# Performance work log

Hardware: AMD Instinct MI355X
Metric: run time of the kernel (lower is better)

Reference implementation:

```python
import jax, jax.numpy as jnp
import numpy as np

SLOPE = 0.2  # LeakyReLU negative slope
EPS = 1e-8


def setup_inputs() -> dict:
    key = jax.random.key(0)
    ks = jax.random.split(key, 10)
    B, LL, D, H = 16, 257, 64, 128
    in_dim = D + 1  # lags=1 -> lags*D + 1
    sc = 0.1
    return {
        "x": jax.random.normal(ks[0], (B, LL, D), dtype=jnp.float32),
        "W1": jax.random.normal(ks[1], (D, H, in_dim), dtype=jnp.float32) * sc,
        "b1": jax.random.normal(ks[2], (D, H), dtype=jnp.float32) * sc,
        "W2": jax.random.normal(ks[3], (D, H, H), dtype=jnp.float32) * sc,
        "b2": jax.random.normal(ks[4], (D, H), dtype=jnp.float32) * sc,
        "W3": jax.random.normal(ks[5], (D, H, H), dtype=jnp.float32) * sc,
        "b3": jax.random.normal(ks[6], (D, H), dtype=jnp.float32) * sc,
        "W4": jax.random.normal(ks[7], (D, 1, H), dtype=jnp.float32) * sc,
        "b4": jax.random.normal(ks[8], (D, 1), dtype=jnp.float32) * sc,
        "lags": 1,
    }


def _forward(x, W1, b1, W2, b2, W3, b3, W4, b4, lags):
    B, LL, D = x.shape
    length = LL - lags
    # sliding windows of size lags+1 along time: [B, length, lags+1, D]
    windows = jnp.stack([x[:, i:i + length] for i in range(lags + 1)], axis=2)
    N = B * length
    x_lags = windows[:, :, :-1].reshape(N, lags * D)  # [N, lags*D]
    x_t = windows[:, :, -1].reshape(N, D)             # [N, D]

    def per_latent(w1, bb1, w2, bb2, w3, bb3, w4, bb4, xti):
        inp = jnp.concatenate([x_lags, xti[:, None]], axis=-1)  # [N, lags*D+1]
        p1 = inp @ w1.T + bb1
        s1 = jnp.where(p1 > 0, 1.0, SLOPE)
        a1 = p1 * s1
        p2 = a1 @ w2.T + bb2
        s2 = jnp.where(p2 > 0, 1.0, SLOPE)
        a2 = p2 * s2
        p3 = a2 @ w3.T + bb3
        s3 = jnp.where(p3 > 0, 1.0, SLOPE)
        a3 = p3 * s3
        out = a3 @ w4.T + bb4  # [N, 1]
        # analytic d out / d x_{t,i} (Jacobian diagonal): chain through LeakyReLU slopes
        d = s1 * w1[:, -1]      # [N, H]
        d = s2 * (d @ w2.T)     # [N, H]
        d = s3 * (d @ w3.T)     # [N, H]
        deriv = d @ w4[0]       # [N]
        return out[:, 0], deriv

    res, deriv = jax.vmap(per_latent, in_axes=(0, 0, 0, 0, 0, 0, 0, 0, 1))(
        W1, b1, W2, b2, W3, b3, W4, b4, x_t)  # res, deriv: [D, N]
    residuals = res.T.reshape(B, length, D)
    log_abs_det = jnp.log(jnp.abs(deriv) + EPS).sum(axis=0).reshape(B, length)
    return residuals, log_abs_det


def reference(x, W1, b1, W2, b2, W3, b3, W4, b4, lags):
    return _forward(x, W1, b1, W2, b2, W3, b3, W4, b4, lags)
```

## Files before the change

### kernel.cpp

```cpp
#include <hip/hip_runtime.h>
#include <hip/hip_bf16.h>
#include <math.h>

typedef _Float16 f16;
typedef _Float16 f16x8 __attribute__((ext_vector_type(8)));
typedef _Float16 f16x4 __attribute__((ext_vector_type(4)));
typedef _Float16 f16x2 __attribute__((ext_vector_type(2)));
typedef float f32x4 __attribute__((ext_vector_type(4)));

#define MFMA(a, b, c) __builtin_amdgcn_mfma_f32_16x16x32_f16((a), (b), (c), 0, 0, 0)

constexpr int Dd = 64;
constexpr int Hh = 128;
constexpr int Nn = 4096;
constexpr int NT = 32;
constexpr float SLP = 0.2f;
constexpr float INV2K = 1.0f / 2048.0f;

constexpr int PD = 81920;
constexpr size_t W1L_OFF = (size_t)Dd * PD * 2;
constexpr size_t WS_NEEDED = W1L_OFF + (size_t)Dd * Hh * 4;

__device__ __forceinline__ int swz(int r, int c) {
  return (r << 7) + ((((c >> 3) ^ (r & 15)) << 3) | (c & 7));
}
__device__ __forceinline__ int swzK64(int r, int c) {
  return (r << 6) + (((((c >> 3) ^ r) & 7) << 3) | (c & 7));
}
__device__ __forceinline__ int swzF(int n, int h) {
  return (n << 7) + ((((h >> 2) ^ n) & 31) << 2) + (h & 3);
}

struct HL { f16 h, l; };
__device__ __forceinline__ HL split(float v) {
  HL r;
  r.h = (f16)v;
  r.l = (f16)((v - (float)r.h) * 2048.0f);
  return r;
}

__device__ __forceinline__ void cp_lds_async(const void* g, void* l, int nbytes, int tid) {
  const int lane = tid & 63, wv = tid >> 6;
  for (int base = wv * 1024; base < nbytes; base += 4096) {
    __builtin_amdgcn_global_load_lds(
        (const __attribute__((address_space(1))) void*)((const char*)g + base + lane * 16),
        (__attribute__((address_space(3))) void*)((char*)l + base), 16, 0, 0);
  }
}

__global__ __launch_bounds__(256)
void prep_kernel(const float* __restrict__ W1, const float* __restrict__ W2,
                 const float* __restrict__ W3, f16* __restrict__ wsf,
                 float* __restrict__ w1lg) {
  const int d = blockIdx.x, sec = blockIdx.y, tid = threadIdx.x;
  f16* out = wsf + (size_t)d * PD;
  if (sec == 0) {
    const float* W1d = W1 + d * Hh * 65;
    for (int ip = tid; ip < 4096; ip += 256) {
      int h = ip >> 5, k2 = (ip & 31) << 1;
      HL a = split(W1d[h * 65 + k2]);
      HL b = split(W1d[h * 65 + k2 + 1]);
      int o = (h >> 6) * 8192 + swzK64(h & 63, k2);
      *(f16x2*)&out[o] = f16x2{a.h, b.h};
      *(f16x2*)&out[o + 4096] = f16x2{a.l, b.l};
    }
    if (tid < 128) w1lg[d * Hh + tid] = W1d[tid * 65 + 64];
  } else {
    int w = (sec - 1) >> 1, hh = (sec - 1) & 1;
    const float* g = (w == 0 ? W2 : W3) + d * Hh * Hh + hh * 8192;
    f16* ob = out + 16384 + w * 32768 + hh * 16384;
    for (int ip = tid; ip < 4096; ip += 256) {
      int h = ip >> 6, k2 = (ip & 63) << 1;
      float2 v = *(const float2*)&g[h * 128 + k2];
      HL a = split(v.x), b = split(v.y);
      int o = swz(h, k2);
      *(f16x2*)&ob[o] = f16x2{a.h, b.h};
      *(f16x2*)&ob[o + 8192] = f16x2{a.l, b.l};
    }
  }
}

__device__ __forceinline__ void mid_mfma_half(
    const f16* AH, const f16* AL, const f16* DH, const f16* DL,
    const f16* WH, const f16* WL, int nt, int wq, int l15, int quad,
    f32x4* aP, f32x4* aS, f32x4* dP, f32x4* dS) {
#pragma unroll
  for (int kc = 0; kc < 4; kc++) {
    int ko = kc * 32 + quad * 8;
    int ra = nt * 16 + l15;
    f16x8 xh = *(const f16x8*)&AH[swz(ra, ko)];
    f16x8 xl = *(const f16x8*)&AL[swz(ra, ko)];
    f16x8 yh = *(const f16x8*)&DH[swz(ra, ko)];
    f16x8 yl = *(const f16x8*)&DL[swz(ra, ko)];
#pragma unroll
    for (int c2 = 0; c2 < 2; c2++) {
      int hr = (2 * wq + c2) * 16 + l15;
      f16x8 wh = *(const f16x8*)&WH[swz(hr, ko)];
      f16x8 wl = *(const f16x8*)&WL[swz(hr, ko)];
      aP[c2] = MFMA(wh, xh, aP[c2]);
      aS[c2] = MFMA(wl, xh, aS[c2]);
      aS[c2] = MFMA(wh, xl, aS[c2]);
      dP[c2] = MFMA(wh, yh, dP[c2]);
      dS[c2] = MFMA(wl, yh, dS[c2]);
      dS[c2] = MFMA(wh, yl, dS[c2]);
    }
  }
}

__global__ __launch_bounds__(256, 2)
void np_prior_fast(const float* __restrict__ x, const f16* __restrict__ wsw,
                   const float* __restrict__ w1lg,
                   const float* __restrict__ b1, const float* __restrict__ b2,
                   const float* __restrict__ b3, const float* __restrict__ W4,
                   const float* __restrict__ b4,
                   float* __restrict__ out_res, float* __restrict__ out_log) {
  __shared__ float4 smem[4096];
  f16* AH = (f16*)smem;
  f16* AL = AH + NT * 128;
  f16* DH = AL + NT * 128;
  f16* DL = DH + NT * 128;
  f16* Wreg = (f16*)((char*)smem + 32768);
  float* A3F = (float*)smem;
  float* D3F = (float*)((char*)smem + 16384);

  const int tid = threadIdx.x, d = blockIdx.y, n0 = blockIdx.x * NT;
  const int lane = tid & 63, wv = tid >> 6, l15 = lane & 15, quad = lane >> 4;
  const int nt = wv & 1, wq = wv >> 1;

  const f16* wd = wsw + (size_t)d * PD;
  const float* w1l = w1lg + d * Hh;
  const float* b1d = b1 + d * Hh;
  const f32x4 zero = {0.f, 0.f, 0.f, 0.f};

  cp_lds_async(wd, Wreg, 16384, tid);

  for (int i = tid; i < NT * 16; i += 256) {
    int n = i >> 4, k4 = (i & 15) << 2;
    int ng = n0 + n, bb = ng >> 8, tt = ng & 255;
    float4 v = *(const float4*)&x[(bb * 257 + tt) * 64 + k4];
    HL a = split(v.x), b = split(v.y), c = split(v.z), e = split(v.w);
    int o = swz(n, k4);
    *(f16x4*)&AH[o] = f16x4{a.h, b.h, c.h, e.h};
    *(f16x4*)&AL[o] = f16x4{a.l, b.l, c.l, e.l};
  }
  float xtv;
  {
    int ng = n0 + nt * 16 + l15, bb = ng >> 8, tt = ng & 255;
    xtv = x[(bb * 257 + tt + 1) * 64 + d];
  }
  __syncthreads();

  f32x4 l1P[2][2], l1S[2][2];
  for (int hf = 0; hf < 2; hf++) {
    if (hf == 1) {
      __syncthreads();
      cp_lds_async(wd + 8192, Wreg, 16384, tid);
      __syncthreads();
    }
    l1P[hf][0] = zero; l1P[hf][1] = zero;
    l1S[hf][0] = zero; l1S[hf][1] = zero;
#pragma unroll
    for (int kc = 0; kc < 2; kc++) {
      int ko = kc * 32 + quad * 8;
      f16x8 xh = *(const f16x8*)&AH[swz(nt * 16 + l15, ko)];
      f16x8 xl = *(const f16x8*)&AL[swz(nt * 16 + l15, ko)];
#pragma unroll
      for (int c2 = 0; c2 < 2; c2++) {
        int hr = (2 * wq + c2) * 16 + l15;
        f16x8 wh = *(const f16x8*)&Wreg[swzK64(hr, ko)];
        f16x8 wl = *(const f16x8*)&Wreg[4096 + swzK64(hr, ko)];
        l1P[hf][c2] = MFMA(wh, xh, l1P[hf][c2]);
        l1S[hf][c2] = MFMA(wl, xh, l1S[hf][c2]);
        l1S[hf][c2] = MFMA(wh, xl, l1S[hf][c2]);
      }
    }
  }
  __syncthreads();
  cp_lds_async(wd + 16384, Wreg, 32768, tid);

  {
    int n = nt * 16 + l15;
#pragma unroll
    for (int hf = 0; hf < 2; hf++)
#pragma unroll
      for (int c2 = 0; c2 < 2; c2++) {
        int hb = hf * 64 + (2 * wq + c2) * 16 + quad * 4;
        float4 wv4 = *(const float4*)&w1l[hb];
        float4 bv4 = *(const float4*)&b1d[hb];
        f16x4 ah, al, dh, dl;
#pragma unroll
        for (int j = 0; j < 4; j++) {
          float w1j = (&wv4.x)[j];
          float p = l1P[hf][c2][j] + l1S[hf][c2][j] * INV2K + xtv * w1j + (&bv4.x)[j];
          float s = p > 0.f ? 1.f : SLP;
          HL av = split(p * s), dv = split(s * w1j);
          ah[j] = av.h; al[j] = av.l; dh[j] = dv.h; dl[j] = dv.l;
        }
        int o = swz(n, hb);
        *(f16x4*)&AH[o] = ah; *(f16x4*)&AL[o] = al;
        *(f16x4*)&DH[o] = dh; *(f16x4*)&DL[o] = dl;
      }
  }
  __syncthreads();

  f32x4 aP[2][2], aS[2][2], dP[2][2], dS[2][2];
  for (int hf = 0; hf < 2; hf++) {
    if (hf == 1) {
      __syncthreads();
      cp_lds_async(wd + 32768, Wreg, 32768, tid);
      __syncthreads();
    }
    aP[hf][0] = zero; aP[hf][1] = zero; aS[hf][0] = zero; aS[hf][1] = zero;
    dP[hf][0] = zero; dP[hf][1] = zero; dS[hf][0] = zero; dS[hf][1] = zero;
    mid_mfma_half(AH, AL, DH, DL, Wreg, Wreg + 8192, nt, wq, l15, quad,
                  aP[hf], aS[hf], dP[hf], dS[hf]);
  }
  __syncthreads();
  cp_lds_async(wd + 49152, Wreg, 32768, tid);

  {
    const float* b2d = b2 + d * Hh;
    int n = nt * 16 + l15;
#pragma unroll
    for (int hf = 0; hf < 2; hf++)
#pragma unroll
      for (int c2 = 0; c2 < 2; c2++) {
        int hb = hf * 64 + (2 * wq + c2) * 16 + quad * 4;
        float4 bv4 = *(const float4*)&b2d[hb];
        f16x4 ah, al, dh, dl;
#pragma unroll
        for (int j = 0; j < 4; j++) {
          float p = aP[hf][c2][j] + aS[hf][c2][j] * INV2K + (&bv4.x)[j];
          float s = p > 0.f ? 1.f : SLP;
          float dd = s * (dP[hf][c2][j] + dS[hf][c2][j] * INV2K);
          HL av = split(p * s), dv = split(dd);
          ah[j] = av.h; al[j] = av.l; dh[j] = dv.h; dl[j] = dv.l;
        }
        int o = swz(n, hb);
        *(f16x4*)&AH[o] = ah; *(f16x4*)&AL[o] = al;
        *(f16x4*)&DH[o] = dh; *(f16x4*)&DL[o] = dl;
      }
  }
  __syncthreads();

  for (int hf = 0; hf < 2; hf++) {
    if (hf == 1) {
      __syncthreads();
      cp_lds_async(wd + 65536, Wreg, 32768, tid);
      __syncthreads();
    }
    aP[hf][0] = zero; aP[hf][1] = zero; aS[hf][0] = zero; aS[hf][1] = zero;
    dP[hf][0] = zero; dP[hf][1] = zero; dS[hf][0] = zero; dS[hf][1] = zero;
    mid_mfma_half(AH, AL, DH, DL, Wreg, Wreg + 8192, nt, wq, l15, quad,
                  aP[hf], aS[hf], dP[hf], dS[hf]);
  }
  __syncthreads();

  {
    const float* b3d = b3 + d * Hh;
    int n = nt * 16 + l15;
#pragma unroll
    for (int hf = 0; hf < 2; hf++)
#pragma unroll
      for (int c2 = 0; c2 < 2; c2++) {
        int hb = hf * 64 + (2 * wq + c2) * 16 + quad * 4;
        float4 bv4 = *(const float4*)&b3d[hb];
        float4 pa, pd;
#pragma unroll
        for (int j = 0; j < 4; j++) {
          float p = aP[hf][c2][j] + aS[hf][c2][j] * INV2K + (&bv4.x)[j];
          float s = p > 0.f ? 1.f : SLP;
          (&pa.x)[j] = p * s;
          (&pd.x)[j] = s * (dP[hf][c2][j] + dS[hf][c2][j] * INV2K);
        }
        *(float4*)&A3F[swzF(n, hb)] = pa;
        *(float4*)&D3F[swzF(n, hb)] = pd;
      }
  }
  __syncthreads();

  {
    int n = tid >> 3, oct = tid & 7;
    const float* w4d = W4 + d * Hh;
    float sr = 0.f, sd = 0.f;
#pragma unroll
    for (int i = 0; i < 4; i++) {
      int c = oct * 16 + i * 4;
      float4 va = *(const float4*)&A3F[swzF(n, c)];
      float4 vd = *(const float4*)&D3F[swzF(n, c)];
      float4 w = *(const float4*)&w4d[c];
      sr += va.x * w.x + va.y * w.y + va.z * w.z + va.w * w.w;
      sd += vd.x * w.x + vd.y * w.y + vd.z * w.z + vd.w * w.w;
    }
    sr += __shfl_xor(sr, 1); sr += __shfl_xor(sr, 2); sr += __shfl_xor(sr, 4);
    sd += __shfl_xor(sd, 1); sd += __shfl_xor(sd, 2); sd += __shfl_xor(sd, 4);
    if (oct == 0) {
      int ng = n0 + n;
      out_res[ng * 64 + d] = sr + b4[d];
      atomicAdd(&out_log[ng], logf(fabsf(sd) + 1e-8f));
    }
  }
}

__device__ __forceinline__ void stage_wf(f16* WH, f16* WL,
                                         const float* __restrict__ g, int tid) {
  for (int i = tid; i < 2048; i += 256) {
    int h = i >> 5, k4 = (i & 31) << 2;
    float4 v = ((const float4*)g)[i];
    HL a = split(v.x), b = split(v.y), c = split(v.z), e = split(v.w);
    int o = swz(h, k4);
    *(f16x4*)&WH[o] = f16x4{a.h, b.h, c.h, e.h};
    *(f16x4*)&WL[o] = f16x4{a.l, b.l, c.l, e.l};
  }
}

__global__ __launch_bounds__(256, 2)
void np_prior_fb(const float* __restrict__ x,
                 const float* __restrict__ W1, const float* __restrict__ b1,
                 const float* __restrict__ W2, const float* __restrict__ b2,
                 const float* __restrict__ W3, const float* __restrict__ b3,
                 const float* __restrict__ W4, const float* __restrict__ b4,
                 float* __restrict__ out_res, float* __restrict__ out_log) {
  __shared__ float4 smem[4096];
  f16* AH = (f16*)smem;
  f16* AL = AH + NT * 128;
  f16* DH = AL + NT * 128;
  f16* DL = DH + NT * 128;
  f16* WHp = (f16*)((char*)smem + 32768);
  f16* WLp = WHp + 64 * 128;
  float* A3F = (float*)smem;
  float* D3F = (float*)((char*)smem + 16384);

  const int tid = threadIdx.x, d = blockIdx.y, n0 = blockIdx.x * NT;
  const int lane = tid & 63, wv = tid >> 6, l15 = lane & 15, quad = lane >> 4;
  const int nt = wv & 1, wq = wv >> 1;

  const float* W1d = W1 + d * Hh * 65;
  const float* b1d = b1 + d * Hh;
  const f32x4 zero = {0.f, 0.f, 0.f, 0.f};

  for (int i = tid; i < NT * 16; i += 256) {
    int n = i >> 4, k4 = (i & 15) << 2;
    int ng = n0 + n, bb = ng >> 8, tt = ng & 255;
    float4 v = *(const float4*)&x[(bb * 257 + tt) * 64 + k4];
    HL a = split(v.x), b = split(v.y), c = split(v.z), e = split(v.w);
    int o = swz(n, k4);
    *(f16x4*)&AH[o] = f16x4{a.h, b.h, c.h, e.h};
    *(f16x4*)&AL[o] = f16x4{a.l, b.l, c.l, e.l};
  }
  float xtv;
  {
    int ng = n0 + nt * 16 + l15, bb = ng >> 8, tt = ng & 255;
    xtv = x[(bb * 257 + tt + 1) * 64 + d];
  }
  for (int i = tid; i < 64 * 64; i += 256) {
    int h = i >> 6, k = i & 63;
    HL s = split(W1d[h * 65 + k]);
    int o = swz(h, k);
    WHp[o] = s.h; WLp[o] = s.l;
  }
  __syncthreads();

  f32x4 l1P[2][2], l1S[2][2];
  for (int hf = 0; hf < 2; hf++) {
    if (hf == 1) {
      __syncthreads();
      for (int i = tid; i < 64 * 64; i += 256) {
        int h = i >> 6, k = i & 63;
        HL s = split(W1d[(64 + h) * 65 + k]);
        int o = swz(h, k);
        WHp[o] = s.h; WLp[o] = s.l;
      }
      __syncthreads();
    }
    l1P[hf][0] = zero; l1P[hf][1] = zero;
    l1S[hf][0] = zero; l1S[hf][1] = zero;
#pragma unroll
    for (int kc = 0; kc < 2; kc++) {
      int ko = kc * 32 + quad * 8;
      f16x8 xh = *(const f16x8*)&AH[swz(nt * 16 + l15, ko)];
      f16x8 xl = *(const f16x8*)&AL[swz(nt * 16 + l15, ko)];
#pragma unroll
      for (int c2 = 0; c2 < 2; c2++) {
        int hr = (2 * wq + c2) * 16 + l15;
        f16x8 wh = *(const f16x8*)&WHp[swz(hr, ko)];
        f16x8 wl = *(const f16x8*)&WLp[swz(hr, ko)];
        l1P[hf][c2] = MFMA(wh, xh, l1P[hf][c2]);
        l1S[hf][c2] = MFMA(wl, xh, l1S[hf][c2]);
        l1S[hf][c2] = MFMA(wh, xl, l1S[hf][c2]);
      }
    }
  }
  __syncthreads();

  {
    int n = nt * 16 + l15;
#pragma unroll
    for (int hf = 0; hf < 2; hf++)
#pragma unroll
      for (int c2 = 0; c2 < 2; c2++) {
        int hb = hf * 64 + (2 * wq + c2) * 16 + quad * 4;
        f16x4 ah, al, dh, dl;
#pragma unroll
        for (int j = 0; j < 4; j++) {
          int h = hb + j;
          float w1j = W1d[h * 65 + 64];
          float p = l1P[hf][c2][j] + l1S[hf][c2][j] * INV2K + xtv * w1j + b1d[h];
          float s = p > 0.f ? 1.f : SLP;
          HL av = split(p * s), dv = split(s * w1j);
          ah[j] = av.h; al[j] = av.l; dh[j] = dv.h; dl[j] = dv.l;
        }
        int o = swz(n, hb);
        *(f16x4*)&AH[o] = ah; *(f16x4*)&AL[o] = al;
        *(f16x4*)&DH[o] = dh; *(f16x4*)&DL[o] = dl;
      }
  }
  stage_wf(WHp, WLp, W2 + d * Hh * Hh, tid);
  __syncthreads();

  f32x4 aP[2][2], aS[2][2], dP[2][2], dS[2][2];
  for (int hf = 0; hf < 2; hf++) {
    if (hf == 1) {
      __syncthreads();
      stage_wf(WHp, WLp, W2 + d * Hh * Hh + 64 * 128, tid);
      __syncthreads();
    }
    aP[hf][0] = zero; aP[hf][1] = zero; aS[hf][0] = zero; aS[hf][1] = zero;
    dP[hf][0] = zero; dP[hf][1] = zero; dS[hf][0] = zero; dS[hf][1] = zero;
    mid_mfma_half(AH, AL, DH, DL, WHp, WLp, nt, wq, l15, quad,
                  aP[hf], aS[hf], dP[hf], dS[hf]);
  }
  __syncthreads();

  {
    const float* b2d = b2 + d * Hh;
    int n = nt * 16 + l15;
#pragma unroll
    for (int hf = 0; hf < 2; hf++)
#pragma unroll
      for (int c2 = 0; c2 < 2; c2++) {
        int hb = hf * 64 + (2 * wq + c2) * 16 + quad * 4;
        f16x4 ah, al, dh, dl;
#pragma unroll
        for (int j = 0; j < 4; j++) {
          int h = hb + j;
          float p = aP[hf][c2][j] + aS[hf][c2][j] * INV2K + b2d[h];
          float s = p > 0.f ? 1.f : SLP;
          float dd = s * (dP[hf][c2][j] + dS[hf][c2][j] * INV2K);
          HL av = split(p * s), dv = split(dd);
          ah[j] = av.h; al[j] = av.l; dh[j] = dv.h; dl[j] = dv.l;
        }
        int o = swz(n, hb);
        *(f16x4*)&AH[o] = ah; *(f16x4*)&AL[o] = al;
        *(f16x4*)&DH[o] = dh; *(f16x4*)&DL[o] = dl;
      }
  }
  stage_wf(WHp, WLp, W3 + d * Hh * Hh, tid);
  __syncthreads();

  for (int hf = 0; hf < 2; hf++) {
    if (hf == 1) {
      __syncthreads();
      stage_wf(WHp, WLp, W3 + d * Hh * Hh + 64 * 128, tid);
      __syncthreads();
    }
    aP[hf][0] = zero; aP[hf][1] = zero; aS[hf][0] = zero; aS[hf][1] = zero;
    dP[hf][0] = zero; dP[hf][1] = zero; dS[hf][0] = zero; dS[hf][1] = zero;
    mid_mfma_half(AH, AL, DH, DL, WHp, WLp, nt, wq, l15, quad,
                  aP[hf], aS[hf], dP[hf], dS[hf]);
  }
  __syncthreads();

  {
    const float* b3d = b3 + d * Hh;
    int n = nt * 16 + l15;
#pragma unroll
    for (int hf = 0; hf < 2; hf++)
#pragma unroll
      for (int c2 = 0; c2 < 2; c2++) {
        int hb = hf * 64 + (2 * wq + c2) * 16 + quad * 4;
        float4 pa, pd;
#pragma unroll
        for (int j = 0; j < 4; j++) {
          int h = hb + j;
          float p = aP[hf][c2][j] + aS[hf][c2][j] * INV2K + b3d[h];
          float s = p > 0.f ? 1.f : SLP;
          (&pa.x)[j] = p * s;
          (&pd.x)[j] = s * (dP[hf][c2][j] + dS[hf][c2][j] * INV2K);
        }
        *(float4*)&A3F[swzF(n, hb)] = pa;
        *(float4*)&D3F[swzF(n, hb)] = pd;
      }
  }
  __syncthreads();

  {
    int n = tid >> 3, oct = tid & 7;
    const float* w4d = W4 + d * Hh;
    float sr = 0.f, sd = 0.f;
#pragma unroll
    for (int i = 0; i < 4; i++) {
      int c = oct * 16 + i * 4;
      float4 va = *(const float4*)&A3F[swzF(n, c)];
      float4 vd = *(const float4*)&D3F[swzF(n, c)];
      float4 w = *(const float4*)&w4d[c];
      sr += va.x * w.x + va.y * w.y + va.z * w.z + va.w * w.w;
      sd += vd.x * w.x + vd.y * w.y + vd.z * w.z + vd.w * w.w;
    }
    sr += __shfl_xor(sr, 1); sr += __shfl_xor(sr, 2); sr += __shfl_xor(sr, 4);
    sd += __shfl_xor(sd, 1); sd += __shfl_xor(sd, 2); sd += __shfl_xor(sd, 4);
    if (oct == 0) {
      int ng = n0 + n;
      out_res[ng * 64 + d] = sr + b4[d];
      atomicAdd(&out_log[ng], logf(fabsf(sd) + 1e-8f));
    }
  }
}

extern "C" void kernel_launch(void* const* d_in, const int* in_sizes, int n_in,
                              void* d_out, int out_size, void* d_ws, size_t ws_size,
                              hipStream_t stream) {
  (void)in_sizes; (void)n_in; (void)out_size;
  const float* x  = (const float*)d_in[0];
  const float* W1 = (const float*)d_in[1];
  const float* b1 = (const float*)d_in[2];
  const float* W2 = (const float*)d_in[3];
  const float* b2 = (const float*)d_in[4];
  const float* W3 = (const float*)d_in[5];
  const float* b3 = (const float*)d_in[6];
  const float* W4 = (const float*)d_in[7];
  const float* b4 = (const float*)d_in[8];

  float* out_res = (float*)d_out;
  float* out_log = out_res + Nn * Dd;
  hipMemsetAsync(out_log, 0, Nn * sizeof(float), stream);

  dim3 grid(Nn / NT, Dd);
  if (ws_size >= WS_NEEDED) {
    f16* wsf = (f16*)d_ws;
    float* w1lg = (float*)((char*)d_ws + W1L_OFF);
    prep_kernel<<<dim3(Dd, 5), 256, 0, stream>>>(W1, W2, W3, wsf, w1lg);
    np_prior_fast<<<grid, 256, 0, stream>>>(x, wsf, w1lg, b1, b2, b3, W4, b4,
                                            out_res, out_log);
  } else {
    np_prior_fb<<<grid, 256, 0, stream>>>(x, W1, b1, W2, b2, W3, b3, W4, b4,
                                          out_res, out_log);
  }
}
```

Before: 253.0 us.

## Keep only high halves in LDS; stream low-half weights from global in fragment order

The prep kernel now writes the high f16 half of each weight matrix in swizzled LDS layout, and the low (residual) half in MFMA fragment order so each lane can load it directly from global/L2 into registers. The main kernel therefore only stages the 32KB high half per layer in LDS. This removes the split-in-two LDS passes and their extra barriers, and each wave now computes all four of its output tiles in one pass. Low-half fragments are software-prefetched one k-chunk ahead, at the cost of more registers and global loads per block.

```diff
diff --git a/kernel.cpp b/kernel.cpp
--- a/kernel.cpp
+++ b/kernel.cpp
@@ -5,7 +5,6 @@
 typedef _Float16 f16;
 typedef _Float16 f16x8 __attribute__((ext_vector_type(8)));
 typedef _Float16 f16x4 __attribute__((ext_vector_type(4)));
-typedef _Float16 f16x2 __attribute__((ext_vector_type(2)));
 typedef float f32x4 __attribute__((ext_vector_type(4)));
 
 #define MFMA(a, b, c) __builtin_amdgcn_mfma_f32_16x16x32_f16((a), (b), (c), 0, 0, 0)
@@ -56,54 +55,92 @@
   f16* out = wsf + (size_t)d * PD;
   if (sec == 0) {
     const float* W1d = W1 + d * Hh * 65;
-    for (int ip = tid; ip < 4096; ip += 256) {
-      int h = ip >> 5, k2 = (ip & 31) << 1;
-      HL a = split(W1d[h * 65 + k2]);
-      HL b = split(W1d[h * 65 + k2 + 1]);
-      int o = (h >> 6) * 8192 + swzK64(h & 63, k2);
-      *(f16x2*)&out[o] = f16x2{a.h, b.h};
-      *(f16x2*)&out[o + 4096] = f16x2{a.l, b.l};
+    for (int fid = tid; fid < 1024; fid += 256) {
+      int r = fid >> 3, chunk = fid & 7;
+      int c0 = (chunk ^ (r & 7)) << 3;
+      f16x8 hv;
+#pragma unroll
+      for (int j = 0; j < 8; j++) hv[j] = (f16)W1d[r * 65 + c0 + j];
+      *(f16x8*)&out[fid * 8] = hv;
+    }
+    for (int fid = tid; fid < 1024; fid += 256) {
+      int lane = fid & 63, kc = (fid >> 6) & 1, t = fid >> 7;
+      int h = t * 16 + (lane & 15), k = kc * 32 + (lane >> 4) * 8;
+      f16x8 lv;
+#pragma unroll
+      for (int j = 0; j < 8; j++) {
+        float v = W1d[h * 65 + k + j];
+        f16 hi = (f16)v;
+        lv[j] = (f16)((v - (float)hi) * 2048.0f);
+      }
+      *(f16x8*)&out[8192 + fid * 8] = lv;
     }
     if (tid < 128) w1lg[d * Hh + tid] = W1d[tid * 65 + 64];
   } else {
-    int w = (sec - 1) >> 1, hh = (sec - 1) & 1;
-    const float* g = (w == 0 ? W2 : W3) + d * Hh * Hh + hh * 8192;
-    f16* ob = out + 16384 + w * 32768 + hh * 16384;
-    for (int ip = tid; ip < 4096; ip += 256) {
-      int h = ip >> 6, k2 = (ip & 63) << 1;
-      float2 v = *(const float2*)&g[h * 128 + k2];
-      HL a = split(v.x), b = split(v.y);
-      int o = swz(h, k2);
-      *(f16x2*)&ob[o] = f16x2{a.h, b.h};
-      *(f16x2*)&ob[o + 8192] = f16x2{a.l, b.l};
-    }
-  }
-}
-
-__device__ __forceinline__ void mid_mfma_half(
+    const float* g = (sec == 1 ? W2 : W3) + d * Hh * Hh;
+    f16* oh = out + (sec == 1 ? 16384 : 49152);
+    f16* ol = out + (sec == 1 ? 32768 : 65536);
+    for (int fid = tid; fid < 2048; fid += 256) {
+      int r = fid >> 4, chunk = fid & 15;
+      int c0 = (chunk ^ (r & 15)) << 3;
+      const float* s = &g[r * 128 + c0];
+      float4 v0 = *(const float4*)s, v1 = *(const float4*)(s + 4);
+      f16x8 hv = {(f16)v0.x, (f16)v0.y, (f16)v0.z, (f16)v0.w,
+                  (f16)v1.x, (f16)v1.y, (f16)v1.z, (f16)v1.w};
+      *(f16x8*)&oh[fid * 8] = hv;
+    }
+    for (int fid = tid; fid < 2048; fid += 256) {
+      int lane = fid & 63, kc = (fid >> 6) & 3, t = fid >> 8;
+      int h = t * 16 + (lane & 15), k = kc * 32 + (lane >> 4) * 8;
+      const float* s = &g[h * 128 + k];
+      float4 v0 = *(const float4*)s, v1 = *(const float4*)(s + 4);
+      float vv[8] = {v0.x, v0.y, v0.z, v0.w, v1.x, v1.y, v1.z, v1.w};
+      f16x8 lv;
+#pragma unroll
+      for (int j = 0; j < 8; j++) {
+        f16 hi = (f16)vv[j];
+        lv[j] = (f16)((vv[j] - (float)hi) * 2048.0f);
+      }
+      *(f16x8*)&ol[fid * 8] = lv;
+    }
+  }
+}
+
+__device__ __forceinline__ void mid_phase(
     const f16* AH, const f16* AL, const f16* DH, const f16* DL,
-    const f16* WH, const f16* WL, int nt, int wq, int l15, int quad,
-    f32x4* aP, f32x4* aS, f32x4* dP, f32x4* dS) {
+    const f16* WHI, const f16* __restrict__ wlo, int nt, int wq, int l15,
+    int quad, int lane, f32x4 (&aP)[4], f32x4 (&aS)[4], f32x4 (&dP)[4],
+    f32x4 (&dS)[4]) {
+  const int ra = nt * 16 + l15;
+  f16x8 loc[4], lon[4];
+#pragma unroll
+  for (int c2 = 0; c2 < 4; c2++)
+    loc[c2] = *(const f16x8*)&wlo[(((wq * 4 + c2) * 4 + 0) * 64 + lane) * 8];
 #pragma unroll
   for (int kc = 0; kc < 4; kc++) {
+    if (kc < 3) {
+#pragma unroll
+      for (int c2 = 0; c2 < 4; c2++)
+        lon[c2] = *(const f16x8*)&wlo[(((wq * 4 + c2) * 4 + kc + 1) * 64 + lane) * 8];
+    }
     int ko = kc * 32 + quad * 8;
-    int ra = nt * 16 + l15;
     f16x8 xh = *(const f16x8*)&AH[swz(ra, ko)];
     f16x8 xl = *(const f16x8*)&AL[swz(ra, ko)];
     f16x8 yh = *(const f16x8*)&DH[swz(ra, ko)];
     f16x8 yl = *(const f16x8*)&DL[swz(ra, ko)];
 #pragma unroll
-    for (int c2 = 0; c2 < 2; c2++) {
-      int hr = (2 * wq + c2) * 16 + l15;
-      f16x8 wh = *(const f16x8*)&WH[swz(hr, ko)];
-      f16x8 wl = *(const f16x8*)&WL[swz(hr, ko)];
+    for (int c2 = 0; c2 < 4; c2++) {
+      int h = (wq * 4 + c2) * 16 + l15;
+      f16x8 wh = *(const f16x8*)&WHI[swz(h, ko)];
       aP[c2] = MFMA(wh, xh, aP[c2]);
-      aS[c2] = MFMA(wl, xh, aS[c2]);
+      aS[c2] = MFMA(loc[c2], xh, aS[c2]);
       aS[c2] = MFMA(wh, xl, aS[c2]);
       dP[c2] = MFMA(wh, yh, dP[c2]);
-      dS[c2] = MFMA(wl, yh, dS[c2]);
+      dS[c2] = MFMA(loc[c2], yh, dS[c2]);
       dS[c2] = MFMA(wh, yl, dS[c2]);
     }
+#pragma unroll
+    for (int c2 = 0; c2 < 4; c2++) loc[c2] = lon[c2];
   }
 }
 
@@ -119,7 +156,7 @@
   f16* AL = AH + NT * 128;
   f16* DH = AL + NT * 128;
   f16* DL = DH + NT * 128;
-  f16* Wreg = (f16*)((char*)smem + 32768);
+  f16* WHI = (f16*)((char*)smem + 32768);
   float* A3F = (float*)smem;
   float* D3F = (float*)((char*)smem + 16384);
 
@@ -132,8 +169,7 @@
   const float* b1d = b1 + d * Hh;
   const f32x4 zero = {0.f, 0.f, 0.f, 0.f};
 
-  cp_lds_async(wd, Wreg, 16384, tid);
-
+  cp_lds_async(wd, WHI, 16384, tid);
   for (int i = tid; i < NT * 16; i += 256) {
     int n = i >> 4, k4 = (i & 15) << 2;
     int ng = n0 + n, bb = ng >> 8, tt = ng & 255;
@@ -150,132 +186,111 @@
   }
   __syncthreads();
 
-  f32x4 l1P[2][2], l1S[2][2];
-  for (int hf = 0; hf < 2; hf++) {
-    if (hf == 1) {
-      __syncthreads();
-      cp_lds_async(wd + 8192, Wreg, 16384, tid);
-      __syncthreads();
-    }
-    l1P[hf][0] = zero; l1P[hf][1] = zero;
-    l1S[hf][0] = zero; l1S[hf][1] = zero;
+  f32x4 aP[4], aS[4], dP[4], dS[4];
+  {
+    const f16* wlo = wd + 8192;
+    const int ra = nt * 16 + l15;
+    f16x8 lo1[4][2];
+#pragma unroll
+    for (int c2 = 0; c2 < 4; c2++)
+#pragma unroll
+      for (int kc = 0; kc < 2; kc++)
+        lo1[c2][kc] = *(const f16x8*)&wlo[(((wq * 4 + c2) * 2 + kc) * 64 + lane) * 8];
+#pragma unroll
+    for (int c2 = 0; c2 < 4; c2++) { aP[c2] = zero; aS[c2] = zero; }
 #pragma unroll
     for (int kc = 0; kc < 2; kc++) {
       int ko = kc * 32 + quad * 8;
-      f16x8 xh = *(const f16x8*)&AH[swz(nt * 16 + l15, ko)];
-      f16x8 xl = *(const f16x8*)&AL[swz(nt * 16 + l15, ko)];
-#pragma unroll
-      for (int c2 = 0; c2 < 2; c2++) {
-        int hr = (2 * wq + c2) * 16 + l15;
-        f16x8 wh = *(const f16x8*)&Wreg[swzK64(hr, ko)];
-        f16x8 wl = *(const f16x8*)&Wreg[4096 + swzK64(hr, ko)];
-        l1P[hf][c2] = MFMA(wh, xh, l1P[hf][c2]);
-        l1S[hf][c2] = MFMA(wl, xh, l1S[hf][c2]);
-        l1S[hf][c2] = MFMA(wh, xl, l1S[hf][c2]);
-      }
-    }
-  }
-  __syncthreads();
-  cp_lds_async(wd + 16384, Wreg, 32768, tid);
+      f16x8 xh = *(const f16x8*)&AH[swz(ra, ko)];
+      f16x8 xl = *(const f16x8*)&AL[swz(ra, ko)];
+#pragma unroll
+      for (int c2 = 0; c2 < 4; c2++) {
+        int h = (wq * 4 + c2) * 16 + l15;
+        f16x8 wh = *(const f16x8*)&WHI[swzK64(h, ko)];
+        aP[c2] = MFMA(wh, xh, aP[c2]);
+        aS[c2] = MFMA(lo1[c2][kc], xh, aS[c2]);
+        aS[c2] = MFMA(wh, xl, aS[c2]);
+      }
+    }
+  }
+  __syncthreads();
+  cp_lds_async(wd + 16384, WHI, 32768, tid);
 
   {
     int n = nt * 16 + l15;
 #pragma unroll
-    for (int hf = 0; hf < 2; hf++)
-#pragma unroll
-      for (int c2 = 0; c2 < 2; c2++) {
-        int hb = hf * 64 + (2 * wq + c2) * 16 + quad * 4;
-        float4 wv4 = *(const float4*)&w1l[hb];
-        float4 bv4 = *(const float4*)&b1d[hb];
-        f16x4 ah, al, dh, dl;
-#pragma unroll
-        for (int j = 0; j < 4; j++) {
-          float w1j = (&wv4.x)[j];
-          float p = l1P[hf][c2][j] + l1S[hf][c2][j] * INV2K + xtv * w1j + (&bv4.x)[j];
-          float s = p > 0.f ? 1.f : SLP;
-          HL av = split(p * s), dv = split(s * w1j);
-          ah[j] = av.h; al[j] = av.l; dh[j] = dv.h; dl[j] = dv.l;
-        }
-        int o = swz(n, hb);
-        *(f16x4*)&AH[o] = ah; *(f16x4*)&AL[o] = al;
-        *(f16x4*)&DH[o] = dh; *(f16x4*)&DL[o] = dl;
-      }
-  }
-  __syncthreads();
-
-  f32x4 aP[2][2], aS[2][2], dP[2][2], dS[2][2];
-  for (int hf = 0; hf < 2; hf++) {
-    if (hf == 1) {
-      __syncthreads();
-      cp_lds_async(wd + 32768, Wreg, 32768, tid);
-      __syncthreads();
-    }
-    aP[hf][0] = zero; aP[hf][1] = zero; aS[hf][0] = zero; aS[hf][1] = zero;
-    dP[hf][0] = zero; dP[hf][1] = zero; dS[hf][0] = zero; dS[hf][1] = zero;
-    mid_mfma_half(AH, AL, DH, DL, Wreg, Wreg + 8192, nt, wq, l15, quad,
-                  aP[hf], aS[hf], dP[hf], dS[hf]);
-  }
-  __syncthreads();
-  cp_lds_async(wd + 49152, Wreg, 32768, tid);
+    for (int c2 = 0; c2 < 4; c2++) {
+      int hb = (wq * 4 + c2) * 16 + quad * 4;
+      float4 wv4 = *(const float4*)&w1l[hb];
+      float4 bv4 = *(const float4*)&b1d[hb];
+      f16x4 ah, al, dh, dl;
+#pragma unroll
+      for (int j = 0; j < 4; j++) {
+        float w1j = (&wv4.x)[j];
+        float p = aP[c2][j] + aS[c2][j] * INV2K + xtv * w1j + (&bv4.x)[j];
+        float s = p > 0.f ? 1.f : SLP;
+        HL av = split(p * s), dv = split(s * w1j);
+        ah[j] = av.h; al[j] = av.l; dh[j] = dv.h; dl[j] = dv.l;
+      }
+      int o = swz(n, hb);
+      *(f16x4*)&AH[o] = ah; *(f16x4*)&AL[o] = al;
+      *(f16x4*)&DH[o] = dh; *(f16x4*)&DL[o] = dl;
+    }
+  }
+  __syncthreads();
+
+#pragma unroll
+  for (int c2 = 0; c2 < 4; c2++) { aP[c2] = zero; aS[c2] = zero; dP[c2] = zero; dS[c2] = zero; }
+  mid_phase(AH, AL, DH, DL, WHI, wd + 32768, nt, wq, l15, quad, lane, aP, aS, dP, dS);
+  __syncthreads();
+  cp_lds_async(wd + 49152, WHI, 32768, tid);
 
   {
     const float* b2d = b2 + d * Hh;
     int n = nt * 16 + l15;
 #pragma unroll
-    for (int hf = 0; hf < 2; hf++)
-#pragma unroll
-      for (int c2 = 0; c2 < 2; c2++) {
-        int hb = hf * 64 + (2 * wq + c2) * 16 + quad * 4;
-        float4 bv4 = *(const float4*)&b2d[hb];
-        f16x4 ah, al, dh, dl;
-#pragma unroll
-        for (int j = 0; j < 4; j++) {
-          float p = aP[hf][c2][j] + aS[hf][c2][j] * INV2K + (&bv4.x)[j];
-          float s = p > 0.f ? 1.f : SLP;
-          float dd = s * (dP[hf][c2][j] + dS[hf][c2][j] * INV2K);
-          HL av = split(p * s), dv = split(dd);
-          ah[j] = av.h; al[j] = av.l; dh[j] = dv.h; dl[j] = dv.l;
-        }
-        int o = swz(n, hb);
-        *(f16x4*)&AH[o] = ah; *(f16x4*)&AL[o] = al;
-        *(f16x4*)&DH[o] = dh; *(f16x4*)&DL[o] = dl;
-      }
-  }
-  __syncthreads();
-
-  for (int hf = 0; hf < 2; hf++) {
-    if (hf == 1) {
-      __syncthreads();
-      cp_lds_async(wd + 65536, Wreg, 32768, tid);
-      __syncthreads();
-    }
-    aP[hf][0] = zero; aP[hf][1] = zero; aS[hf][0] = zero; aS[hf][1] = zero;
-    dP[hf][0] = zero; dP[hf][1] = zero; dS[hf][0] = zero; dS[hf][1] = zero;
-    mid_mfma_half(AH, AL, DH, DL, Wreg, Wreg + 8192, nt, wq, l15, quad,
-                  aP[hf], aS[hf], dP[hf], dS[hf]);
-  }
+    for (int c2 = 0; c2 < 4; c2++) {
+      int hb = (wq * 4 + c2) * 16 + quad * 4;
+      float4 bv4 = *(const float4*)&b2d[hb];
+      f16x4 ah, al, dh, dl;
+#pragma unroll
+      for (int j = 0; j < 4; j++) {
+        float p = aP[c2][j] + aS[c2][j] * INV2K + (&bv4.x)[j];
+        float s = p > 0.f ? 1.f : SLP;
+        float dd = s * (dP[c2][j] + dS[c2][j] * INV2K);
+        HL av = split(p * s), dv = split(dd);
+        ah[j] = av.h; al[j] = av.l; dh[j] = dv.h; dl[j] = dv.l;
+      }
+      int o = swz(n, hb);
+      *(f16x4*)&AH[o] = ah; *(f16x4*)&AL[o] = al;
+      *(f16x4*)&DH[o] = dh; *(f16x4*)&DL[o] = dl;
+    }
+  }
+  __syncthreads();
+
+#pragma unroll
+  for (int c2 = 0; c2 < 4; c2++) { aP[c2] = zero; aS[c2] = zero; dP[c2] = zero; dS[c2] = zero; }
+  mid_phase(AH, AL, DH, DL, WHI, wd + 65536, nt, wq, l15, quad, lane, aP, aS, dP, dS);
   __syncthreads();
 
   {
     const float* b3d = b3 + d * Hh;
     int n = nt * 16 + l15;
 #pragma unroll
-    for (int hf = 0; hf < 2; hf++)
-#pragma unroll
-      for (int c2 = 0; c2 < 2; c2++) {
-        int hb = hf * 64 + (2 * wq + c2) * 16 + quad * 4;
-        float4 bv4 = *(const float4*)&b3d[hb];
-        float4 pa, pd;
-#pragma unroll
-        for (int j = 0; j < 4; j++) {
-          float p = aP[hf][c2][j] + aS[hf][c2][j] * INV2K + (&bv4.x)[j];
-          float s = p > 0.f ? 1.f : SLP;
-          (&pa.x)[j] = p * s;
-          (&pd.x)[j] = s * (dP[hf][c2][j] + dS[hf][c2][j] * INV2K);
-        }
-        *(float4*)&A3F[swzF(n, hb)] = pa;
-        *(float4*)&D3F[swzF(n, hb)] = pd;
-      }
+    for (int c2 = 0; c2 < 4; c2++) {
+      int hb = (wq * 4 + c2) * 16 + quad * 4;
+      float4 bv4 = *(const float4*)&b3d[hb];
+      float4 pa, pd;
+#pragma unroll
+      for (int j = 0; j < 4; j++) {
+        float p = aP[c2][j] + aS[c2][j] * INV2K + (&bv4.x)[j];
+        float s = p > 0.f ? 1.f : SLP;
+        (&pa.x)[j] = p * s;
+        (&pd.x)[j] = s * (dP[c2][j] + dS[c2][j] * INV2K);
+      }
+      *(float4*)&A3F[swzF(n, hb)] = pa;
+      *(float4*)&D3F[swzF(n, hb)] = pd;
+    }
   }
   __syncthreads();
 
@@ -311,6 +326,33 @@
     int o = swz(h, k4);
     *(f16x4*)&WH[o] = f16x4{a.h, b.h, c.h, e.h};
     *(f16x4*)&WL[o] = f16x4{a.l, b.l, c.l, e.l};
+  }
+}
+
+__device__ __forceinline__ void mid_mfma_half(
+    const f16* AH, const f16* AL, const f16* DH, const f16* DL,
+    const f16* WH, const f16* WL, int nt, int wq, int l15, int quad,
+    f32x4* aP, f32x4* aS, f32x4* dP, f32x4* dS) {
+#pragma unroll
+  for (int kc = 0; kc < 4; kc++) {
+    int ko = kc * 32 + quad * 8;
+    int ra = nt * 16 + l15;
+    f16x8 xh = *(const f16x8*)&AH[swz(ra, ko)];
+    f16x8 xl = *(const f16x8*)&AL[swz(ra, ko)];
+    f16x8 yh = *(const f16x8*)&DH[swz(ra, ko)];
+    f16x8 yl = *(const f16x8*)&DL[swz(ra, ko)];
+#pragma unroll
+    for (int c2 = 0; c2 < 2; c2++) {
+      int hr = (2 * wq + c2) * 16 + l15;
+      f16x8 wh = *(const f16x8*)&WH[swz(hr, ko)];
+      f16x8 wl = *(const f16x8*)&WL[swz(hr, ko)];
+      aP[c2] = MFMA(wh, xh, aP[c2]);
+      aS[c2] = MFMA(wl, xh, aS[c2]);
+      aS[c2] = MFMA(wh, xl, aS[c2]);
+      dP[c2] = MFMA(wh, yh, dP[c2]);
+      dS[c2] = MFMA(wl, yh, dS[c2]);
+      dS[c2] = MFMA(wh, yl, dS[c2]);
+    }
   }
 }
 
@@ -539,7 +581,7 @@
   if (ws_size >= WS_NEEDED) {
     f16* wsf = (f16*)d_ws;
     float* w1lg = (float*)((char*)d_ws + W1L_OFF);
-    prep_kernel<<<dim3(Dd, 5), 256, 0, stream>>>(W1, W2, W3, wsf, w1lg);
+    prep_kernel<<<dim3(Dd, 3), 256, 0, stream>>>(W1, W2, W3, wsf, w1lg);
     np_prior_fast<<<grid, 256, 0, stream>>>(x, wsf, w1lg, b1, b2, b3, W4, b4,
                                             out_res, out_log);
   } else {
```

Result: slower. 286.7 us (+13.3%).

## Double block size to 512 threads, one 16x16 tile per wave, fold memset into prep

Applied to the files above, without the earlier changes.

The fast kernel now launches 512 threads per block, so each of the 8 waves owns a single 16-row hidden tile instead of two. That halves the accumulators held per thread and raises the occupancy target in launch bounds. The async LDS copy stride, input staging and final W4 reduction are reworked to match the larger block. The out_log zeroing moves from a separate hipMemsetAsync into prep_kernel to save a launch. The cost is that each wave issues fewer MFMAs between the weight and activation loads it shares, so there is less reuse per wave.

```diff
diff --git a/kernel.cpp b/kernel.cpp
--- a/kernel.cpp
+++ b/kernel.cpp
@@ -39,9 +39,9 @@
   return r;
 }
 
-__device__ __forceinline__ void cp_lds_async(const void* g, void* l, int nbytes, int tid) {
+__device__ __forceinline__ void cp_lds_async512(const void* g, void* l, int nbytes, int tid) {
   const int lane = tid & 63, wv = tid >> 6;
-  for (int base = wv * 1024; base < nbytes; base += 4096) {
+  for (int base = wv * 1024; base < nbytes; base += 8192) {
     __builtin_amdgcn_global_load_lds(
         (const __attribute__((address_space(1))) void*)((const char*)g + base + lane * 16),
         (__attribute__((address_space(3))) void*)((char*)l + base), 16, 0, 0);
@@ -51,7 +51,7 @@
 __global__ __launch_bounds__(256)
 void prep_kernel(const float* __restrict__ W1, const float* __restrict__ W2,
                  const float* __restrict__ W3, f16* __restrict__ wsf,
-                 float* __restrict__ w1lg) {
+                 float* __restrict__ w1lg, float* __restrict__ out_log) {
   const int d = blockIdx.x, sec = blockIdx.y, tid = threadIdx.x;
   f16* out = wsf + (size_t)d * PD;
   if (sec == 0) {
@@ -65,6 +65,7 @@
       *(f16x2*)&out[o + 4096] = f16x2{a.l, b.l};
     }
     if (tid < 128) w1lg[d * Hh + tid] = W1d[tid * 65 + 64];
+    if (tid < 64) out_log[d * 64 + tid] = 0.f;
   } else {
     int w = (sec - 1) >> 1, hh = (sec - 1) & 1;
     const float* g = (w == 0 ? W2 : W3) + d * Hh * Hh + hh * 8192;
@@ -80,34 +81,29 @@
   }
 }
 
-__device__ __forceinline__ void mid_mfma_half(
+__device__ __forceinline__ void mid_half(
     const f16* AH, const f16* AL, const f16* DH, const f16* DL,
-    const f16* WH, const f16* WL, int nt, int wq, int l15, int quad,
-    f32x4* aP, f32x4* aS, f32x4* dP, f32x4* dS) {
+    const f16* WH, const f16* WL, int ra, int hr, int quad,
+    f32x4& aP, f32x4& aS, f32x4& dP, f32x4& dS) {
 #pragma unroll
   for (int kc = 0; kc < 4; kc++) {
     int ko = kc * 32 + quad * 8;
-    int ra = nt * 16 + l15;
     f16x8 xh = *(const f16x8*)&AH[swz(ra, ko)];
     f16x8 xl = *(const f16x8*)&AL[swz(ra, ko)];
     f16x8 yh = *(const f16x8*)&DH[swz(ra, ko)];
     f16x8 yl = *(const f16x8*)&DL[swz(ra, ko)];
-#pragma unroll
-    for (int c2 = 0; c2 < 2; c2++) {
-      int hr = (2 * wq + c2) * 16 + l15;
-      f16x8 wh = *(const f16x8*)&WH[swz(hr, ko)];
-      f16x8 wl = *(const f16x8*)&WL[swz(hr, ko)];
-      aP[c2] = MFMA(wh, xh, aP[c2]);
-      aS[c2] = MFMA(wl, xh, aS[c2]);
-      aS[c2] = MFMA(wh, xl, aS[c2]);
-      dP[c2] = MFMA(wh, yh, dP[c2]);
-      dS[c2] = MFMA(wl, yh, dS[c2]);
-      dS[c2] = MFMA(wh, yl, dS[c2]);
-    }
-  }
-}
-
-__global__ __launch_bounds__(256, 2)
+    f16x8 wh = *(const f16x8*)&WH[swz(hr, ko)];
+    f16x8 wl = *(const f16x8*)&WL[swz(hr, ko)];
+    aP = MFMA(wh, xh, aP);
+    aS = MFMA(wl, xh, aS);
+    aS = MFMA(wh, xl, aS);
+    dP = MFMA(wh, yh, dP);
+    dS = MFMA(wl, yh, dS);
+    dS = MFMA(wh, yl, dS);
+  }
+}
+
+__global__ __launch_bounds__(512, 4)
 void np_prior_fast(const float* __restrict__ x, const f16* __restrict__ wsw,
                    const float* __restrict__ w1lg,
                    const float* __restrict__ b1, const float* __restrict__ b2,
@@ -126,16 +122,17 @@
   const int tid = threadIdx.x, d = blockIdx.y, n0 = blockIdx.x * NT;
   const int lane = tid & 63, wv = tid >> 6, l15 = lane & 15, quad = lane >> 4;
   const int nt = wv & 1, wq = wv >> 1;
+  const int ra = nt * 16 + l15;
+  const int hr = wq * 16 + l15;
 
   const f16* wd = wsw + (size_t)d * PD;
   const float* w1l = w1lg + d * Hh;
   const float* b1d = b1 + d * Hh;
   const f32x4 zero = {0.f, 0.f, 0.f, 0.f};
 
-  cp_lds_async(wd, Wreg, 16384, tid);
-
-  for (int i = tid; i < NT * 16; i += 256) {
-    int n = i >> 4, k4 = (i & 15) << 2;
+  cp_lds_async512(wd, Wreg, 16384, tid);
+  {
+    int n = tid >> 4, k4 = (tid & 15) << 2;
     int ng = n0 + n, bb = ng >> 8, tt = ng & 255;
     float4 v = *(const float4*)&x[(bb * 257 + tt) * 64 + k4];
     HL a = split(v.x), b = split(v.y), c = split(v.z), e = split(v.w);
@@ -145,156 +142,144 @@
   }
   float xtv;
   {
-    int ng = n0 + nt * 16 + l15, bb = ng >> 8, tt = ng & 255;
+    int ng = n0 + ra, bb = ng >> 8, tt = ng & 255;
     xtv = x[(bb * 257 + tt + 1) * 64 + d];
   }
   __syncthreads();
 
-  f32x4 l1P[2][2], l1S[2][2];
+  f32x4 l1P[2], l1S[2];
+#pragma unroll
   for (int hf = 0; hf < 2; hf++) {
     if (hf == 1) {
       __syncthreads();
-      cp_lds_async(wd + 8192, Wreg, 16384, tid);
-      __syncthreads();
-    }
-    l1P[hf][0] = zero; l1P[hf][1] = zero;
-    l1S[hf][0] = zero; l1S[hf][1] = zero;
+      cp_lds_async512(wd + 8192, Wreg, 16384, tid);
+      __syncthreads();
+    }
+    l1P[hf] = zero; l1S[hf] = zero;
 #pragma unroll
     for (int kc = 0; kc < 2; kc++) {
       int ko = kc * 32 + quad * 8;
-      f16x8 xh = *(const f16x8*)&AH[swz(nt * 16 + l15, ko)];
-      f16x8 xl = *(const f16x8*)&AL[swz(nt * 16 + l15, ko)];
-#pragma unroll
-      for (int c2 = 0; c2 < 2; c2++) {
-        int hr = (2 * wq + c2) * 16 + l15;
-        f16x8 wh = *(const f16x8*)&Wreg[swzK64(hr, ko)];
-        f16x8 wl = *(const f16x8*)&Wreg[4096 + swzK64(hr, ko)];
-        l1P[hf][c2] = MFMA(wh, xh, l1P[hf][c2]);
-        l1S[hf][c2] = MFMA(wl, xh, l1S[hf][c2]);
-        l1S[hf][c2] = MFMA(wh, xl, l1S[hf][c2]);
-      }
-    }
-  }
-  __syncthreads();
-  cp_lds_async(wd + 16384, Wreg, 32768, tid);
-
-  {
-    int n = nt * 16 + l15;
-#pragma unroll
-    for (int hf = 0; hf < 2; hf++)
-#pragma unroll
-      for (int c2 = 0; c2 < 2; c2++) {
-        int hb = hf * 64 + (2 * wq + c2) * 16 + quad * 4;
-        float4 wv4 = *(const float4*)&w1l[hb];
-        float4 bv4 = *(const float4*)&b1d[hb];
-        f16x4 ah, al, dh, dl;
-#pragma unroll
-        for (int j = 0; j < 4; j++) {
-          float w1j = (&wv4.x)[j];
-          float p = l1P[hf][c2][j] + l1S[hf][c2][j] * INV2K + xtv * w1j + (&bv4.x)[j];
-          float s = p > 0.f ? 1.f : SLP;
-          HL av = split(p * s), dv = split(s * w1j);
-          ah[j] = av.h; al[j] = av.l; dh[j] = dv.h; dl[j] = dv.l;
-        }
-        int o = swz(n, hb);
-        *(f16x4*)&AH[o] = ah; *(f16x4*)&AL[o] = al;
-        *(f16x4*)&DH[o] = dh; *(f16x4*)&DL[o] = dl;
-      }
-  }
-  __syncthreads();
-
-  f32x4 aP[2][2], aS[2][2], dP[2][2], dS[2][2];
+      f16x8 xh = *(const f16x8*)&AH[swz(ra, ko)];
+      f16x8 xl = *(const f16x8*)&AL[swz(ra, ko)];
+      f16x8 wh = *(const f16x8*)&Wreg[swzK64(hr, ko)];
+      f16x8 wl = *(const f16x8*)&Wreg[4096 + swzK64(hr, ko)];
+      l1P[hf] = MFMA(wh, xh, l1P[hf]);
+      l1S[hf] = MFMA(wl, xh, l1S[hf]);
+      l1S[hf] = MFMA(wh, xl, l1S[hf]);
+    }
+  }
+  __syncthreads();
+  cp_lds_async512(wd + 16384, Wreg, 32768, tid);
+
+#pragma unroll
+  for (int hf = 0; hf < 2; hf++) {
+    int hb = hf * 64 + wq * 16 + quad * 4;
+    float4 wv4 = *(const float4*)&w1l[hb];
+    float4 bv4 = *(const float4*)&b1d[hb];
+    f16x4 ah, al, dh, dl;
+#pragma unroll
+    for (int j = 0; j < 4; j++) {
+      float w1j = (&wv4.x)[j];
+      float p = l1P[hf][j] + l1S[hf][j] * INV2K + xtv * w1j + (&bv4.x)[j];
+      float s = p > 0.f ? 1.f : SLP;
+      HL av = split(p * s), dv = split(s * w1j);
+      ah[j] = av.h; al[j] = av.l; dh[j] = dv.h; dl[j] = dv.l;
+    }
+    int o = swz(ra, hb);
+    *(f16x4*)&AH[o] = ah; *(f16x4*)&AL[o] = al;
+    *(f16x4*)&DH[o] = dh; *(f16x4*)&DL[o] = dl;
+  }
+  __syncthreads();
+
+  f32x4 aP[2], aS[2], dP[2], dS[2];
+#pragma unroll
   for (int hf = 0; hf < 2; hf++) {
     if (hf == 1) {
       __syncthreads();
-      cp_lds_async(wd + 32768, Wreg, 32768, tid);
-      __syncthreads();
-    }
-    aP[hf][0] = zero; aP[hf][1] = zero; aS[hf][0] = zero; aS[hf][1] = zero;
-    dP[hf][0] = zero; dP[hf][1] = zero; dS[hf][0] = zero; dS[hf][1] = zero;
-    mid_mfma_half(AH, AL, DH, DL, Wreg, Wreg + 8192, nt, wq, l15, quad,
-                  aP[hf], aS[hf], dP[hf], dS[hf]);
-  }
-  __syncthreads();
-  cp_lds_async(wd + 49152, Wreg, 32768, tid);
+      cp_lds_async512(wd + 32768, Wreg, 32768, tid);
+      __syncthreads();
+    }
+    aP[hf] = zero; aS[hf] = zero; dP[hf] = zero; dS[hf] = zero;
+    mid_half(AH, AL, DH, DL, Wreg, Wreg + 8192, ra, hr, quad,
+             aP[hf], aS[hf], dP[hf], dS[hf]);
+  }
+  __syncthreads();
+  cp_lds_async512(wd + 49152, Wreg, 32768, tid);
 
   {
     const float* b2d = b2 + d * Hh;
-    int n = nt * 16 + l15;
-#pragma unroll
-    for (int hf = 0; hf < 2; hf++)
-#pragma unroll
-      for (int c2 = 0; c2 < 2; c2++) {
-        int hb = hf * 64 + (2 * wq + c2) * 16 + quad * 4;
-        float4 bv4 = *(const float4*)&b2d[hb];
-        f16x4 ah, al, dh, dl;
-#pragma unroll
-        for (int j = 0; j < 4; j++) {
-          float p = aP[hf][c2][j] + aS[hf][c2][j] * INV2K + (&bv4.x)[j];
-          float s = p > 0.f ? 1.f : SLP;
-          float dd = s * (dP[hf][c2][j] + dS[hf][c2][j] * INV2K);
-          HL av = split(p * s), dv = split(dd);
-          ah[j] = av.h; al[j] = av.l; dh[j] = dv.h; dl[j] = dv.l;
-        }
-        int o = swz(n, hb);
-        *(f16x4*)&AH[o] = ah; *(f16x4*)&AL[o] = al;
-        *(f16x4*)&DH[o] = dh; *(f16x4*)&DL[o] = dl;
-      }
-  }
-  __syncthreads();
-
+#pragma unroll
+    for (int hf = 0; hf < 2; hf++) {
+      int hb = hf * 64 + wq * 16 + quad * 4;
+      float4 bv4 = *(const float4*)&b2d[hb];
+      f16x4 ah, al, dh, dl;
+#pragma unroll
+      for (int j = 0; j < 4; j++) {
+        float p = aP[hf][j] + aS[hf][j] * INV2K + (&bv4.x)[j];
+        float s = p > 0.f ? 1.f : SLP;
+        float dd = s * (dP[hf][j] + dS[hf][j] * INV2K);
+        HL av = split(p * s), dv = split(dd);
+        ah[j] = av.h; al[j] = av.l; dh[j] = dv.h; dl[j] = dv.l;
+      }
+      int o = swz(ra, hb);
+      *(f16x4*)&AH[o] = ah; *(f16x4*)&AL[o] = al;
+      *(f16x4*)&DH[o] = dh; *(f16x4*)&DL[o] = dl;
+    }
+  }
+  __syncthreads();
+
+#pragma unroll
   for (int hf = 0; hf < 2; hf++) {
     if (hf == 1) {
       __syncthreads();
-      cp_lds_async(wd + 65536, Wreg, 32768, tid);
-      __syncthreads();
-    }
-    aP[hf][0] = zero; aP[hf][1] = zero; aS[hf][0] = zero; aS[hf][1] = zero;
-    dP[hf][0] = zero; dP[hf][1] = zero; dS[hf][0] = zero; dS[hf][1] = zero;
-    mid_mfma_half(AH, AL, DH, DL, Wreg, Wreg + 8192, nt, wq, l15, quad,
-                  aP[hf], aS[hf], dP[hf], dS[hf]);
+      cp_lds_async512(wd + 65536, Wreg, 32768, tid);
+      __syncthreads();
+    }
+    aP[hf] = zero; aS[hf] = zero; dP[hf] = zero; dS[hf] = zero;
+    mid_half(AH, AL, DH, DL, Wreg, Wreg + 8192, ra, hr, quad,
+             aP[hf], aS[hf], dP[hf], dS[hf]);
   }
   __syncthreads();
 
   {
     const float* b3d = b3 + d * Hh;
-    int n = nt * 16 + l15;
-#pragma unroll
-    for (int hf = 0; hf < 2; hf++)
-#pragma unroll
-      for (int c2 = 0; c2 < 2; c2++) {
-        int hb = hf * 64 + (2 * wq + c2) * 16 + quad * 4;
-        float4 bv4 = *(const float4*)&b3d[hb];
-        float4 pa, pd;
-#pragma unroll
-        for (int j = 0; j < 4; j++) {
-          float p = aP[hf][c2][j] + aS[hf][c2][j] * INV2K + (&bv4.x)[j];
-          float s = p > 0.f ? 1.f : SLP;
-          (&pa.x)[j] = p * s;
-          (&pd.x)[j] = s * (dP[hf][c2][j] + dS[hf][c2][j] * INV2K);
-        }
-        *(float4*)&A3F[swzF(n, hb)] = pa;
-        *(float4*)&D3F[swzF(n, hb)] = pd;
-      }
-  }
-  __syncthreads();
-
-  {
-    int n = tid >> 3, oct = tid & 7;
+#pragma unroll
+    for (int hf = 0; hf < 2; hf++) {
+      int hb = hf * 64 + wq * 16 + quad * 4;
+      float4 bv4 = *(const float4*)&b3d[hb];
+      float4 pa, pd;
+#pragma unroll
+      for (int j = 0; j < 4; j++) {
+        float p = aP[hf][j] + aS[hf][j] * INV2K + (&bv4.x)[j];
+        float s = p > 0.f ? 1.f : SLP;
+        (&pa.x)[j] = p * s;
+        (&pd.x)[j] = s * (dP[hf][j] + dS[hf][j] * INV2K);
+      }
+      *(float4*)&A3F[swzF(ra, hb)] = pa;
+      *(float4*)&D3F[swzF(ra, hb)] = pd;
+    }
+  }
+  __syncthreads();
+
+  {
+    int n = tid >> 4, g16 = tid & 15;
     const float* w4d = W4 + d * Hh;
-    float sr = 0.f, sd = 0.f;
-#pragma unroll
-    for (int i = 0; i < 4; i++) {
-      int c = oct * 16 + i * 4;
-      float4 va = *(const float4*)&A3F[swzF(n, c)];
-      float4 vd = *(const float4*)&D3F[swzF(n, c)];
-      float4 w = *(const float4*)&w4d[c];
-      sr += va.x * w.x + va.y * w.y + va.z * w.z + va.w * w.w;
-      sd += vd.x * w.x + vd.y * w.y + vd.z * w.z + vd.w * w.w;
-    }
-    sr += __shfl_xor(sr, 1); sr += __shfl_xor(sr, 2); sr += __shfl_xor(sr, 4);
-    sd += __shfl_xor(sd, 1); sd += __shfl_xor(sd, 2); sd += __shfl_xor(sd, 4);
-    if (oct == 0) {
+    int c = g16 * 8;
+    float4 va0 = *(const float4*)&A3F[swzF(n, c)];
+    float4 va1 = *(const float4*)&A3F[swzF(n, c + 4)];
+    float4 vd0 = *(const float4*)&D3F[swzF(n, c)];
+    float4 vd1 = *(const float4*)&D3F[swzF(n, c + 4)];
+    float4 w0 = *(const float4*)&w4d[c];
+    float4 w1 = *(const float4*)&w4d[c + 4];
+    float sr = va0.x * w0.x + va0.y * w0.y + va0.z * w0.z + va0.w * w0.w +
+               va1.x * w1.x + va1.y * w1.y + va1.z * w1.z + va1.w * w1.w;
+    float sd = vd0.x * w0.x + vd0.y * w0.y + vd0.z * w0.z + vd0.w * w0.w +
+               vd1.x * w1.x + vd1.y * w1.y + vd1.z * w1.z + vd1.w * w1.w;
+    sr += __shfl_xor(sr, 1); sr += __shfl_xor(sr, 2);
+    sr += __shfl_xor(sr, 4); sr += __shfl_xor(sr, 8);
+    sd += __shfl_xor(sd, 1); sd += __shfl_xor(sd, 2);
+    sd += __shfl_xor(sd, 4); sd += __shfl_xor(sd, 8);
+    if (g16 == 0) {
       int ng = n0 + n;
       out_res[ng * 64 + d] = sr + b4[d];
       atomicAdd(&out_log[ng], logf(fabsf(sd) + 1e-8f));
@@ -311,6 +296,33 @@
     int o = swz(h, k4);
     *(f16x4*)&WH[o] = f16x4{a.h, b.h, c.h, e.h};
     *(f16x4*)&WL[o] = f16x4{a.l, b.l, c.l, e.l};
+  }
+}
+
+__device__ __forceinline__ void mid_mfma_half(
+    const f16* AH, const f16* AL, const f16* DH, const f16* DL,
+    const f16* WH, const f16* WL, int nt, int wq, int l15, int quad,
+    f32x4* aP, f32x4* aS, f32x4* dP, f32x4* dS) {
+#pragma unroll
+  for (int kc = 0; kc < 4; kc++) {
+    int ko = kc * 32 + quad * 8;
+    int ra = nt * 16 + l15;
+    f16x8 xh = *(const f16x8*)&AH[swz(ra, ko)];
+    f16x8 xl = *(const f16x8*)&AL[swz(ra, ko)];
+    f16x8 yh = *(const f16x8*)&DH[swz(ra, ko)];
+    f16x8 yl = *(const f16x8*)&DL[swz(ra, ko)];
+#pragma unroll
+    for (int c2 = 0; c2 < 2; c2++) {
+      int hr = (2 * wq + c2) * 16 + l15;
+      f16x8 wh = *(const f16x8*)&WH[swz(hr, ko)];
+      f16x8 wl = *(const f16x8*)&WL[swz(hr, ko)];
+      aP[c2] = MFMA(wh, xh, aP[c2]);
+      aS[c2] = MFMA(wl, xh, aS[c2]);
+      aS[c2] = MFMA(wh, xl, aS[c2]);
+      dP[c2] = MFMA(wh, yh, dP[c2]);
+      dS[c2] = MFMA(wl, yh, dS[c2]);
+      dS[c2] = MFMA(wh, yl, dS[c2]);
+    }
   }
 }
 
@@ -533,16 +545,16 @@
 
   float* out_res = (float*)d_out;
   float* out_log = out_res + Nn * Dd;
-  hipMemsetAsync(out_log, 0, Nn * sizeof(float), stream);
 
   dim3 grid(Nn / NT, Dd);
   if (ws_size >= WS_NEEDED) {
     f16* wsf = (f16*)d_ws;
     float* w1lg = (float*)((char*)d_ws + W1L_OFF);
-    prep_kernel<<<dim3(Dd, 5), 256, 0, stream>>>(W1, W2, W3, wsf, w1lg);
-    np_prior_fast<<<grid, 256, 0, stream>>>(x, wsf, w1lg, b1, b2, b3, W4, b4,
+    prep_kernel<<<dim3(Dd, 5), 256, 0, stream>>>(W1, W2, W3, wsf, w1lg, out_log);
+    np_prior_fast<<<grid, 512, 0, stream>>>(x, wsf, w1lg, b1, b2, b3, W4, b4,
                                             out_res, out_log);
   } else {
+    hipMemsetAsync(out_log, 0, Nn * sizeof(float), stream);
     np_prior_fb<<<grid, 256, 0, stream>>>(x, W1, b1, W2, b2, W3, b3, W4, b4,
                                           out_res, out_log);
   }
```

Measured after the change: 248.0 us. About the same (-2.0%).
